# Kernel tuning notes

Measured on AMD Instinct MI355X. Metric: run time of the kernel, lower is better.

Reference implementation:

```python
import jax, jax.numpy as jnp
from jax import lax
import numpy as np

B, N, NF, EF, MD = 16, 128, 9, 3, 5
H, D, FF, L, O = 24, 768, 3072, 12, 128
NA, NID, NOD, NE, NS, NED = 4608, 256, 256, 1536, 512, 128
S = N + 1
EPS = 1e-5


def setup_inputs() -> dict:
    key = jax.random.key(0)
    ks = iter(jax.random.split(key, 64))
    emb_s = 0.02
    lin_s = 0.02 / np.sqrt(L)

    def nrm(shape, s):
        return jax.random.normal(next(ks), shape, jnp.float32) * s

    inp = {
        'x': jax.random.randint(next(ks), (B, N, NF), 0, NA + 1),
        'in_degree': jax.random.randint(next(ks), (B, N), 0, NID),
        'out_degree': jax.random.randint(next(ks), (B, N), 0, NOD),
        'spatial_pos': jax.random.randint(next(ks), (B, N, N), 0, NS),
        'edge_input': jax.random.randint(next(ks), (B, N, N, MD, EF), 0, NE + 1),
        'attn_bias': jnp.zeros((B, S, S), jnp.float32),
        # embeddings (padding_idx=0 rows zeroed)
        'atom_emb': nrm((NA + 1, D), emb_s).at[0].set(0.0),
        'in_deg_emb': nrm((NID, D), emb_s).at[0].set(0.0),
        'out_deg_emb': nrm((NOD, D), emb_s).at[0].set(0.0),
        'graph_token': nrm((1, D), emb_s),
        'edge_emb': nrm((NE + 1, H), emb_s).at[0].set(0.0),
        'edge_dis_emb': nrm((NED, H, H), emb_s),
        'spatial_emb': nrm((NS, H), emb_s).at[0].set(0.0),
        'virt_dist': nrm((1, H), emb_s),
        # stacked per-layer params
        'ln1_g': jnp.ones((L, D)), 'ln1_b': jnp.zeros((L, D)),
        'wq': nrm((L, D, D), lin_s), 'bq': jnp.zeros((L, D)),
        'wk': nrm((L, D, D), lin_s), 'bk': jnp.zeros((L, D)),
        'wv': nrm((L, D, D), lin_s), 'bv': jnp.zeros((L, D)),
        'wo': nrm((L, D, D), lin_s), 'bo': jnp.zeros((L, D)),
        'ln2_g': jnp.ones((L, D)), 'ln2_b': jnp.zeros((L, D)),
        'w1': nrm((L, D, FF), lin_s), 'b1': jnp.zeros((L, FF)),
        'w2': nrm((L, FF, D), lin_s), 'b2': jnp.zeros((L, D)),
        'final_g': jnp.ones((D,)), 'final_b': jnp.zeros((D,)),
        'out_w': nrm((D, O), lin_s), 'out_b': jnp.zeros((O,)),
    }
    return inp


def _ln(v, g, b):
    m = v.mean(-1, keepdims=True)
    va = ((v - m) ** 2).mean(-1, keepdims=True)
    return (v - m) / jnp.sqrt(va + EPS) * g + b


def _forward(x, in_degree, out_degree, spatial_pos, edge_input, attn_bias,
             atom_emb, in_deg_emb, out_deg_emb, graph_token,
             edge_emb, edge_dis_emb, spatial_emb, virt_dist,
             ln1_g, ln1_b, wq, bq, wk, bk, wv, bv, wo, bo,
             ln2_g, ln2_b, w1, b1, w2, b2, final_g, final_b, out_w, out_b):
    nb = x.shape[0]
    # ---- graph attn bias ----
    # spatial bias [B,H,N,N]
    sp_bias = spatial_emb[spatial_pos].transpose(0, 3, 1, 2)
    # multi-hop edge bias
    sp_ = jnp.where(spatial_pos == 0, 1, spatial_pos)
    sp_ = jnp.where(sp_ > 1, sp_ - 1, sp_)
    sp_ = jnp.clip(sp_, 0, MD)
    ei = edge_emb[edge_input].mean(-2)                       # [B,N,N,MD,H]
    eo = jnp.einsum('bijdh,dhk->bijk', ei, edge_dis_emb[:MD])
    edge_bias = (eo / sp_[..., None].astype(jnp.float32)).transpose(0, 3, 1, 2)
    t = virt_dist.reshape(1, H, 1)                           # virtual-token distance
    gab = jnp.repeat(attn_bias[:, None], H, axis=1)          # [B,H,S,S]
    gab = gab.at[:, :, 1:, 1:].add(sp_bias + edge_bias)
    gab = gab.at[:, :, 1:, 0].add(t)
    gab = gab.at[:, :, 0, :].add(t)
    gab = gab + attn_bias[:, None]
    # ---- node features ----
    nf = atom_emb[x].sum(-2) + in_deg_emb[in_degree] + out_deg_emb[out_degree]
    h = jnp.concatenate([jnp.broadcast_to(graph_token[None], (nb, 1, D)), nf], axis=1)  # [B,S,D]
    dk = D // H
    scale = dk ** -0.5

    def step(hc, p):
        (g1, b1n, Wq, Bq, Wk, Bk, Wv, Bv, Wo, Bo, g2, b2n, W1, B1, W2, B2) = p
        y = _ln(hc, g1, b1n)
        q = (y @ Wq + Bq).reshape(nb, S, H, dk).transpose(0, 2, 1, 3) * scale
        k = (y @ Wk + Bk).reshape(nb, S, H, dk).transpose(0, 2, 1, 3)
        v = (y @ Wv + Bv).reshape(nb, S, H, dk).transpose(0, 2, 1, 3)
        att = jnp.einsum('bhqd,bhkd->bhqk', q, k) + gab
        att = jax.nn.softmax(att, axis=-1)
        ctx = jnp.einsum('bhqk,bhkd->bhqd', att, v)
        ctx = ctx.transpose(0, 2, 1, 3).reshape(nb, S, D)
        hc = hc + (ctx @ Wo + Bo)
        y = _ln(hc, g2, b2n)
        y = jax.nn.gelu(y @ W1 + B1, approximate=False) @ W2 + B2
        return hc + y, None

    h, _ = lax.scan(step, h, (ln1_g, ln1_b, wq, bq, wk, bk, wv, bv, wo, bo,
                              ln2_g, ln2_b, w1, b1, w2, b2))
    h = _ln(h, final_g, final_b)
    return h[:, 0] @ out_w + out_b  # [B,O]


def reference(x, in_degree, out_degree, spatial_pos, edge_input, attn_bias,
              atom_emb, in_deg_emb, out_deg_emb, graph_token,
              edge_emb, edge_dis_emb, spatial_emb, virt_dist,
              ln1_g, ln1_b, wq, bq, wk, bk, wv, bv, wo, bo,
              ln2_g, ln2_b, w1, b1, w2, b2, final_g, final_b, out_w, out_b):
    return _forward(x, in_degree, out_degree, spatial_pos, edge_input, attn_bias,
                    atom_emb, in_deg_emb, out_deg_emb, graph_token,
                    edge_emb, edge_dis_emb, spatial_emb, virt_dist,
                    ln1_g, ln1_b, wq, bq, wk, bk, wv, bv, wo, bo,
                    ln2_g, ln2_b, w1, b1, w2, b2, final_g, final_b, out_w, out_b)
```

## Files before the change

kernel.cpp:

```cpp
#include <hip/hip_runtime.h>
#include <hip/hip_bf16.h>
#include <math.h>

typedef __hip_bfloat16 bf16;
typedef __attribute__((ext_vector_type(8))) short short8;
typedef __attribute__((ext_vector_type(4))) short short4v;
typedef __attribute__((ext_vector_type(4))) float f32x4;

constexpr int NB = 16;
constexpr int ND = 128;
constexpr int SQ = 129;
constexpr int NH = 24;
constexpr int DM = 768;
constexpr int DF = 3072;
constexpr int NLAY = 12;
constexpr int MROWS = NB * SQ;

__device__ __forceinline__ short f2bs(float f) {
  bf16 h = __float2bfloat16(f);
  return *(short*)&h;
}

__device__ __forceinline__ void gload16(const void* g, void* lds) {
  __builtin_amdgcn_global_load_lds(
      (const __attribute__((address_space(1))) unsigned int*)g,
      (__attribute__((address_space(3))) unsigned int*)lds, 16, 0, 0);
}

__global__ void k_nodefeat(const int* __restrict__ x, const int* __restrict__ ind,
                           const int* __restrict__ outd,
                           const float* __restrict__ atom, const float* __restrict__ ide,
                           const float* __restrict__ ode, const float* __restrict__ gtok,
                           float* __restrict__ h) {
  int bs = blockIdx.x;
  int b = bs / SQ, s = bs % SQ;
  int t = threadIdx.x;
  float* hrow = h + (size_t)bs * DM;
  if (s == 0) {
    for (int c = t; c < DM; c += 256) hrow[c] = gtok[c];
  } else {
    int n = s - 1;
    const int* xr = x + (b * ND + n) * 9;
    int a0 = xr[0], a1 = xr[1], a2 = xr[2], a3 = xr[3], a4 = xr[4];
    int a5 = xr[5], a6 = xr[6], a7 = xr[7], a8 = xr[8];
    int ii = ind[b * ND + n], oo = outd[b * ND + n];
    for (int c = t; c < DM; c += 256) {
      float acc = ide[(size_t)ii * DM + c] + ode[(size_t)oo * DM + c];
      acc += atom[(size_t)a0 * DM + c];
      acc += atom[(size_t)a1 * DM + c];
      acc += atom[(size_t)a2 * DM + c];
      acc += atom[(size_t)a3 * DM + c];
      acc += atom[(size_t)a4 * DM + c];
      acc += atom[(size_t)a5 * DM + c];
      acc += atom[(size_t)a6 * DM + c];
      acc += atom[(size_t)a7 * DM + c];
      acc += atom[(size_t)a8 * DM + c];
      hrow[c] = acc;
    }
  }
}

__global__ void k_gab_border(const float* __restrict__ ab, const float* __restrict__ virt,
                             float* __restrict__ gab) {
  int b = blockIdx.x;
  const int tot = NH * SQ + NH * ND;
  for (int idx = threadIdx.x; idx < tot; idx += 256) {
    if (idx < NH * SQ) {
      int hh = idx / SQ, j = idx % SQ;
      float v = 2.f * ab[((size_t)b * SQ + 0) * SQ + j] + virt[hh];
      gab[(((size_t)b * NH + hh) * SQ + 0) * SQ + j] = v;
    } else {
      int r = idx - NH * SQ;
      int hh = r / ND, i = r % ND + 1;
      float v = 2.f * ab[((size_t)b * SQ + i) * SQ + 0] + virt[hh];
      gab[(((size_t)b * NH + hh) * SQ + i) * SQ + 0] = v;
    }
  }
}

__global__ __launch_bounds__(256) void k_gab_edge(
    const int* __restrict__ spos, const int* __restrict__ eidx,
    const float* __restrict__ eemb, const float* __restrict__ edemb,
    const float* __restrict__ semb, const float* __restrict__ ab,
    float* __restrict__ gab) {
  __shared__ int eidxs[960];
  __shared__ short ei2[64 * 136];
  __shared__ short edT[32 * 136];
  __shared__ float ot[24][65];
  __shared__ float rinvA[64], a2A[64];
  __shared__ int spA[64];
  int bi = blockIdx.x;
  int half = bi & 1;
  int i = (bi >> 1) & 127;
  int b = bi >> 8;
  int j0 = half * 64;
  int t = threadIdx.x;
  const size_t rowbase = ((size_t)(b * ND + i)) * ND + j0;

  const int* esrc = eidx + rowbase * 15;
  for (int idx = t; idx < 960; idx += 256) eidxs[idx] = esrc[idx];
  for (int u = t; u < 720; u += 256) {
    int dh = u / 6, kq = u % 6;
    f32x4 v = *(const f32x4*)&edemb[dh * 24 + kq * 4];
    edT[(kq * 4 + 0) * 136 + dh] = f2bs(v[0]);
    edT[(kq * 4 + 1) * 136 + dh] = f2bs(v[1]);
    edT[(kq * 4 + 2) * 136 + dh] = f2bs(v[2]);
    edT[(kq * 4 + 3) * 136 + dh] = f2bs(v[3]);
  }
  for (int u = t; u < 1472; u += 256) {
    int k, dh;
    if (u < 384) { k = u >> 4; dh = 120 + (u & 15); }
    else { int v = u - 384; k = 24 + v / 136; dh = v % 136; }
    edT[k * 136 + dh] = 0;
  }
  if (t < 64) {
    int j = t;
    int sp = spos[rowbase + j];
    int spc = (sp == 0) ? 1 : sp;
    spc = (spc > 1) ? spc - 1 : spc;
    if (spc > 5) spc = 5;
    spA[j] = sp;
    rinvA[j] = 1.f / (float)spc;
    a2A[j] = 2.f * ab[((size_t)b * SQ + (i + 1)) * SQ + (j0 + j + 1)];
  }
  __syncthreads();

  {
    int j = t & 63, d = t >> 6;
#pragma unroll
    for (int pass = 0; pass < 2; pass++) {
      if (pass == 1) {
        if (t >= 64) break;
        j = t; d = 4;
      }
      const int* ep = &eidxs[j * 15 + d * 3];
      const float* r0 = eemb + (size_t)ep[0] * NH;
      const float* r1 = eemb + (size_t)ep[1] * NH;
      const float* r2 = eemb + (size_t)ep[2] * NH;
#pragma unroll
      for (int hq = 0; hq < 6; hq++) {
        f32x4 s = (*(const f32x4*)&r0[hq * 4] + *(const f32x4*)&r1[hq * 4] +
                   *(const f32x4*)&r2[hq * 4]) * (1.f / 3.f);
        short4v o;
        o[0] = f2bs(s[0]); o[1] = f2bs(s[1]); o[2] = f2bs(s[2]); o[3] = f2bs(s[3]);
        *(short4v*)&ei2[j * 136 + d * 24 + hq * 4] = o;
      }
    }
  }
  for (int idx = t; idx < 64 * 8; idx += 256) {
    int j = idx >> 3;
    ei2[j * 136 + 120 + (idx & 7)] = 0;
  }
  __syncthreads();

  int lane = t & 63, w = t >> 6;
  int fr = lane & 15, q = lane >> 4, fo = q * 8;
  f32x4 acc0 = {0.f, 0.f, 0.f, 0.f}, acc1 = {0.f, 0.f, 0.f, 0.f};
#pragma unroll
  for (int kk = 0; kk < 4; kk++) {
    short8 af = *(const short8*)&ei2[(w * 16 + fr) * 136 + kk * 32 + fo];
    short8 b0 = *(const short8*)&edT[(fr) * 136 + kk * 32 + fo];
    short8 b1 = *(const short8*)&edT[(16 + fr) * 136 + kk * 32 + fo];
    acc0 = __builtin_amdgcn_mfma_f32_16x16x32_bf16(af, b0, acc0, 0, 0, 0);
    acc1 = __builtin_amdgcn_mfma_f32_16x16x32_bf16(af, b1, acc1, 0, 0, 0);
  }
#pragma unroll
  for (int e = 0; e < 4; e++) {
    int j = w * 16 + q * 4 + e;
    ot[fr][j] = acc0[e];
    if (fr < 8) ot[16 + fr][j] = acc1[e];
  }
  __syncthreads();
  size_t obase = (((size_t)b * NH) * SQ + (i + 1)) * SQ + (j0 + 1);
  for (int idx = t; idx < 24 * 64; idx += 256) {
    int k = idx >> 6, j = idx & 63;
    float v = a2A[j] + semb[spA[j] * NH + k] + ot[k][j] * rinvA[j];
    gab[obase + (size_t)k * SQ * SQ + j] = v;
  }
}

struct Ptrs4 { const float* p[4]; };

template <int NW>
__global__ void k_transpose(Ptrs4 ps, short* __restrict__ dst, int R, int C,
                            size_t sstride) {
  __shared__ short tile[64][68];
  int z = blockIdx.z;
  const float* src = ps.p[z % NW] + (size_t)(z / NW) * sstride;
  short* d = dst + (size_t)z * (size_t)R * C;
  int r0 = blockIdx.x * 64, c0 = blockIdx.y * 64;
  int t = threadIdx.x;
  int tr = t >> 4, tc = (t & 15) * 4;
#pragma unroll
  for (int i = 0; i < 4; i++) {
    int r = tr + i * 16;
    f32x4 v = *(const f32x4*)(src + (size_t)(r0 + r) * C + c0 + tc);
    tile[r][tc + 0] = f2bs(v[0]);
    tile[r][tc + 1] = f2bs(v[1]);
    tile[r][tc + 2] = f2bs(v[2]);
    tile[r][tc + 3] = f2bs(v[3]);
  }
  __syncthreads();
#pragma unroll
  for (int i = 0; i < 4; i++) {
    int rr = tr + i * 16;
    short4v o;
    o[0] = tile[tc + 0][rr];
    o[1] = tile[tc + 1][rr];
    o[2] = tile[tc + 2][rr];
    o[3] = tile[tc + 3][rr];
    *(short4v*)(d + (size_t)(c0 + rr) * R + r0 + tc) = o;
  }
}

__global__ void k_ln(const float* __restrict__ h, const float* __restrict__ g,
                     const float* __restrict__ bb, bf16* __restrict__ y) {
  int r = blockIdx.x;
  int t = threadIdx.x, lane = t & 63, wid = t >> 6;
  __shared__ float red[8];
  const float* row = h + (size_t)r * DM;
  float v0 = row[t], v1 = row[t + 256], v2 = row[t + 512];
  float s = v0 + v1 + v2;
#pragma unroll
  for (int o = 32; o > 0; o >>= 1) s += __shfl_xor(s, o);
  if (lane == 0) red[wid] = s;
  __syncthreads();
  float mean = (red[0] + red[1] + red[2] + red[3]) * (1.f / 768.f);
  float d0 = v0 - mean, d1 = v1 - mean, d2 = v2 - mean;
  float q = d0 * d0 + d1 * d1 + d2 * d2;
#pragma unroll
  for (int o = 32; o > 0; o >>= 1) q += __shfl_xor(q, o);
  if (lane == 0) red[4 + wid] = q;
  __syncthreads();
  float var = (red[4] + red[5] + red[6] + red[7]) * (1.f / 768.f);
  float rstd = rsqrtf(var + 1e-5f);
  bf16* yr = y + (size_t)r * DM;
  yr[t] = __float2bfloat16(d0 * rstd * g[t] + bb[t]);
  yr[t + 256] = __float2bfloat16(d1 * rstd * g[t + 256] + bb[t + 256]);
  yr[t + 512] = __float2bfloat16(d2 * rstd * g[t + 512] + bb[t + 512]);
}

__global__ void k_ln_add2(float* __restrict__ h, const float* __restrict__ p0,
                          const float* __restrict__ p1, const float* __restrict__ cb,
                          const float* __restrict__ g, const float* __restrict__ bb,
                          bf16* __restrict__ y) {
  int r = blockIdx.x;
  int t = threadIdx.x, lane = t & 63, wid = t >> 6;
  __shared__ float red[8];
  size_t base = (size_t)r * DM;
  float v0 = h[base + t] + p0[base + t] + p1[base + t] + cb[t];
  float v1 = h[base + t + 256] + p0[base + t + 256] + p1[base + t + 256] + cb[t + 256];
  float v2 = h[base + t + 512] + p0[base + t + 512] + p1[base + t + 512] + cb[t + 512];
  h[base + t] = v0;
  h[base + t + 256] = v1;
  h[base + t + 512] = v2;
  float s = v0 + v1 + v2;
#pragma unroll
  for (int o = 32; o > 0; o >>= 1) s += __shfl_xor(s, o);
  if (lane == 0) red[wid] = s;
  __syncthreads();
  float mean = (red[0] + red[1] + red[2] + red[3]) * (1.f / 768.f);
  float d0 = v0 - mean, d1 = v1 - mean, d2 = v2 - mean;
  float q = d0 * d0 + d1 * d1 + d2 * d2;
#pragma unroll
  for (int o = 32; o > 0; o >>= 1) q += __shfl_xor(q, o);
  if (lane == 0) red[4 + wid] = q;
  __syncthreads();
  float var = (red[4] + red[5] + red[6] + red[7]) * (1.f / 768.f);
  float rstd = rsqrtf(var + 1e-5f);
  bf16* yr = y + base;
  yr[t] = __float2bfloat16(d0 * rstd * g[t] + bb[t]);
  yr[t + 256] = __float2bfloat16(d1 * rstd * g[t + 256] + bb[t + 256]);
  yr[t + 512] = __float2bfloat16(d2 * rstd * g[t + 512] + bb[t + 512]);
}

struct GemmPtrs {
  const short* bt[3];
  const float* bias[3];
  void* out[3];
  int aoff[3];
};

template <int MODE>
__device__ __forceinline__ void gemm_store(void* outp, size_t idx, float v) {
  if (MODE == 0 || MODE == 3) {
    ((float*)outp)[idx] = v;
  } else if (MODE == 4) {
    ((bf16*)outp)[idx] = __float2bfloat16(v);
  } else {
    float gg = 0.5f * v * (1.f + erff(v * 0.70710678118654752f));
    ((bf16*)outp)[idx] = __float2bfloat16(gg);
  }
}

template <int MODE>
__global__ __launch_bounds__(256, 2) void k_gemm128(const short* __restrict__ A, GemmPtrs p,
                                                    int M, int N, int K, int lda, int ldb) {
  __shared__ short At[2][128 * 64];
  __shared__ short Bt[2][128 * 64];
  int z = blockIdx.z;
  const short* BT = p.bt[z];
  const float* bias = p.bias[z];
  A += p.aoff[z];
  int m0 = blockIdx.x * 128, n0 = blockIdx.y * 128;
  int t = threadIdx.x, lane = t & 63, wid = t >> 6;
  int wr = wid >> 1, wc = wid & 1;
  f32x4 acc[4][4];
#pragma unroll
  for (int a = 0; a < 4; a++)
#pragma unroll
    for (int c = 0; c < 4; c++) acc[a][c] = (f32x4){0.f, 0.f, 0.f, 0.f};

  int lrow8 = lane >> 3;
  int lseg = (lane & 7) ^ lrow8;
  const short* gA[4];
  const short* gB[4];
#pragma unroll
  for (int i = 0; i < 4; i++) {
    int ar = m0 + wid * 32 + i * 8 + lrow8;
    if (ar >= M) ar = M - 1;
    gA[i] = A + (size_t)ar * lda + lseg * 8;
    int br = n0 + wid * 32 + i * 8 + lrow8;
    gB[i] = BT + (size_t)br * ldb + lseg * 8;
  }

  const int NIT = K >> 6;
#pragma unroll
  for (int i = 0; i < 4; i++) {
    gload16(gA[i], &At[0][(wid * 32 + i * 8) * 64]);
    gload16(gB[i], &Bt[0][(wid * 32 + i * 8) * 64]);
  }
  __syncthreads();

  int fr = lane & 15, q = lane >> 4;
  for (int it = 0; it < NIT; ++it) {
    int cur = it & 1;
    if (it + 1 < NIT) {
      int nxt = cur ^ 1;
      int k0 = (it + 1) << 6;
#pragma unroll
      for (int i = 0; i < 4; i++) {
        gload16(gA[i] + k0, &At[nxt][(wid * 32 + i * 8) * 64]);
        gload16(gB[i] + k0, &Bt[nxt][(wid * 32 + i * 8) * 64]);
      }
    }
    const short* Ab = At[cur];
    const short* Bb = Bt[cur];
#pragma unroll
    for (int kk = 0; kk < 2; kk++) {
      int sg = ((q + kk * 4) ^ (fr & 7)) * 8;
      short8 af[4], bf[4];
#pragma unroll
      for (int mr = 0; mr < 4; mr++)
        af[mr] = *(const short8*)&Ab[(wr * 64 + mr * 16 + fr) * 64 + sg];
#pragma unroll
      for (int nc = 0; nc < 4; nc++)
        bf[nc] = *(const short8*)&Bb[(wc * 64 + nc * 16 + fr) * 64 + sg];
#pragma unroll
      for (int mr = 0; mr < 4; mr++)
#pragma unroll
        for (int nc = 0; nc < 4; nc++)
          acc[mr][nc] = __builtin_amdgcn_mfma_f32_16x16x32_bf16(af[mr], bf[nc], acc[mr][nc], 0, 0, 0);
    }
    __syncthreads();
  }

  int rsub = q * 4;
#pragma unroll
  for (int nc = 0; nc < 4; nc++) {
    int col = n0 + wc * 64 + nc * 16 + fr;
    float bv = (MODE == 3) ? 0.f : bias[col];
#pragma unroll
    for (int mr = 0; mr < 4; mr++) {
#pragma unroll
      for (int e = 0; e < 4; e++) {
        int r = m0 + wr * 64 + mr * 16 + rsub + e;
        if (r < M) gemm_store<MODE>(p.out[z], (size_t)r * N + col, acc[mr][nc][e] + bv);
      }
    }
  }
}

template <int MODE>
__global__ __launch_bounds__(256, 3) void k_gemm64(const short* __restrict__ A, GemmPtrs p,
                                                   int M, int N, int K, int lda, int ldb) {
  __shared__ short At[2][64 * 64];
  __shared__ short Bt[2][128 * 64];
  int z = blockIdx.z;
  const short* BT = p.bt[z];
  const float* bias = p.bias[z];
  A += p.aoff[z];
  int m0 = blockIdx.x * 64, n0 = blockIdx.y * 128;
  int t = threadIdx.x, lane = t & 63, wid = t >> 6;
  int wr = wid >> 1, wc = wid & 1;
  f32x4 acc[2][4];
#pragma unroll
  for (int a = 0; a < 2; a++)
#pragma unroll
    for (int c = 0; c < 4; c++) acc[a][c] = (f32x4){0.f, 0.f, 0.f, 0.f};

  int lrow8 = lane >> 3;
  int lseg = (lane & 7) ^ lrow8;
  const short* gA[2];
  const short* gB[4];
#pragma unroll
  for (int i = 0; i < 2; i++) {
    int ar = m0 + wid * 16 + i * 8 + lrow8;
    if (ar >= M) ar = M - 1;
    gA[i] = A + (size_t)ar * lda + lseg * 8;
  }
#pragma unroll
  for (int i = 0; i < 4; i++) {
    int br = n0 + wid * 32 + i * 8 + lrow8;
    gB[i] = BT + (size_t)br * ldb + lseg * 8;
  }

  const int NIT = K >> 6;
#pragma unroll
  for (int i = 0; i < 2; i++) gload16(gA[i], &At[0][(wid * 16 + i * 8) * 64]);
#pragma unroll
  for (int i = 0; i < 4; i++) gload16(gB[i], &Bt[0][(wid * 32 + i * 8) * 64]);
  __syncthreads();

  int fr = lane & 15, q = lane >> 4;
  for (int it = 0; it < NIT; ++it) {
    int cur = it & 1;
    if (it + 1 < NIT) {
      int nxt = cur ^ 1;
      int k0 = (it + 1) << 6;
#pragma unroll
      for (int i = 0; i < 2; i++) gload16(gA[i] + k0, &At[nxt][(wid * 16 + i * 8) * 64]);
#pragma unroll
      for (int i = 0; i < 4; i++) gload16(gB[i] + k0, &Bt[nxt][(wid * 32 + i * 8) * 64]);
    }
    const short* Ab = At[cur];
    const short* Bb = Bt[cur];
#pragma unroll
    for (int kk = 0; kk < 2; kk++) {
      int sg = ((q + kk * 4) ^ (fr & 7)) * 8;
      short8 af[2], bf[4];
#pragma unroll
      for (int mr = 0; mr < 2; mr++)
        af[mr] = *(const short8*)&Ab[(wr * 32 + mr * 16 + fr) * 64 + sg];
#pragma unroll
      for (int nc = 0; nc < 4; nc++)
        bf[nc] = *(const short8*)&Bb[(wc * 64 + nc * 16 + fr) * 64 + sg];
#pragma unroll
      for (int mr = 0; mr < 2; mr++)
#pragma unroll
        for (int nc = 0; nc < 4; nc++)
          acc[mr][nc] = __builtin_amdgcn_mfma_f32_16x16x32_bf16(af[mr], bf[nc], acc[mr][nc], 0, 0, 0);
    }
    __syncthreads();
  }

  int rsub = q * 4;
#pragma unroll
  for (int nc = 0; nc < 4; nc++) {
    int col = n0 + wc * 64 + nc * 16 + fr;
    float bv = (MODE == 3) ? 0.f : bias[col];
#pragma unroll
    for (int mr = 0; mr < 2; mr++) {
#pragma unroll
      for (int e = 0; e < 4; e++) {
        int r = m0 + wr * 32 + mr * 16 + rsub + e;
        if (r < M) gemm_store<MODE>(p.out[z], (size_t)r * N + col, acc[mr][nc][e] + bv);
      }
    }
  }
}

__global__ __launch_bounds__(256) void k_attn(const bf16* __restrict__ Q,
                                              const bf16* __restrict__ Kb,
                                              const bf16* __restrict__ Vb,
                                              const float* __restrict__ gab,
                                              bf16* __restrict__ ctx) {
  __shared__ short Ql[144 * 40];
  __shared__ short Kl[144 * 40];
  __shared__ short Vt[32 * 168];
  __shared__ short Pc[144 * 40];
  int bh = blockIdx.x;
  int b = bh / NH, hh = bh % NH;
  int t = threadIdx.x;
  for (int idx = t; idx < 32 * 40; idx += 256) {
    int d = idx / 40, kk = 128 + (idx % 40);
    Vt[d * 168 + kk] = 0;
  }
  for (int idx = t; idx < 129 * 4; idx += 256) {
    int s = idx >> 2, seg = idx & 3;
    size_t src = ((size_t)(b * SQ + s)) * DM + hh * 32 + seg * 8;
    *(short8*)&Ql[s * 40 + seg * 8] = *(const short8*)((const short*)Q + src);
    *(short8*)&Kl[s * 40 + seg * 8] = *(const short8*)((const short*)Kb + src);
  }
  for (int idx = t; idx < 15 * 4; idx += 256) {
    int s = 129 + (idx >> 2), seg = idx & 3;
    short8 zz = {0, 0, 0, 0, 0, 0, 0, 0};
    *(short8*)&Ql[s * 40 + seg * 8] = zz;
    *(short8*)&Kl[s * 40 + seg * 8] = zz;
  }
  for (int idx = t; idx < 129 * 4; idx += 256) {
    int kk = idx >> 2, seg = idx & 3;
    size_t src = ((size_t)(b * SQ + kk)) * DM + hh * 32 + seg * 8;
    short8 v = *(const short8*)((const short*)Vb + src);
#pragma unroll
    for (int j = 0; j < 8; j++) Vt[(seg * 8 + j) * 168 + kk] = v[j];
  }
  __syncthreads();

  int lane = t & 63, w = t >> 6;
  int c16 = lane & 15, q4 = lane >> 4;
  const float scale = 0.17677669529663689f;
  const float* gabp = gab + (((size_t)(b * NH + hh)) * SQ) * SQ;

  for (int mt = w; mt < 9; mt += 4) {
    f32x4 sc[9];
    short8 aq = *(const short8*)&Ql[(mt * 16 + c16) * 40 + q4 * 8];
#pragma unroll
    for (int nt = 0; nt < 9; nt++) {
      short8 bk = *(const short8*)&Kl[(nt * 16 + c16) * 40 + q4 * 8];
      f32x4 zz = {0.f, 0.f, 0.f, 0.f};
      sc[nt] = __builtin_amdgcn_mfma_f32_16x16x32_bf16(aq, bk, zz, 0, 0, 0);
    }
#pragma unroll
    for (int e = 0; e < 4; e++) {
      int row = mt * 16 + q4 * 4 + e;
      int rr = row < 129 ? row : 128;
      const float* grow = gabp + (size_t)rr * SQ;
      float mloc = -1e30f;
#pragma unroll
      for (int nt = 0; nt < 9; nt++) {
        int col = nt * 16 + c16;
        float s = (col < 129) ? (sc[nt][e] * scale + grow[col]) : -1e30f;
        sc[nt][e] = s;
        mloc = fmaxf(mloc, s);
      }
#pragma unroll
      for (int o = 1; o < 16; o <<= 1) mloc = fmaxf(mloc, __shfl_xor(mloc, o));
      float sum = 0.f;
#pragma unroll
      for (int nt = 0; nt < 9; nt++) {
        float pp = __expf(sc[nt][e] - mloc);
        sc[nt][e] = pp;
        sum += pp;
      }
#pragma unroll
      for (int o = 1; o < 16; o <<= 1) sum += __shfl_xor(sum, o);
      float inv = 1.f / sum;
#pragma unroll
      for (int nt = 0; nt < 9; nt++) sc[nt][e] *= inv;
    }
    f32x4 oacc0 = {0.f, 0.f, 0.f, 0.f}, oacc1 = {0.f, 0.f, 0.f, 0.f};
#pragma unroll
    for (int c = 0; c < 5; c++) {
#pragma unroll
      for (int u = 0; u < 2; u++) {
        int nt = c * 2 + u;
        if (nt < 9) {
#pragma unroll
          for (int e = 0; e < 4; e++)
            Pc[(mt * 16 + q4 * 4 + e) * 40 + u * 16 + c16] = f2bs(sc[nt][e]);
        } else {
#pragma unroll
          for (int e = 0; e < 4; e++)
            Pc[(mt * 16 + q4 * 4 + e) * 40 + u * 16 + c16] = 0;
        }
      }
      asm volatile("s_waitcnt lgkmcnt(0)" ::: "memory");
      __builtin_amdgcn_sched_barrier(0);
      short8 ap = *(const short8*)&Pc[(mt * 16 + c16) * 40 + q4 * 8];
      short8 bv0 = *(const short8*)&Vt[(c16) * 168 + c * 32 + q4 * 8];
      short8 bv1 = *(const short8*)&Vt[(16 + c16) * 168 + c * 32 + q4 * 8];
      oacc0 = __builtin_amdgcn_mfma_f32_16x16x32_bf16(ap, bv0, oacc0, 0, 0, 0);
      oacc1 = __builtin_amdgcn_mfma_f32_16x16x32_bf16(ap, bv1, oacc1, 0, 0, 0);
    }
#pragma unroll
    for (int e = 0; e < 4; e++) {
      int row = mt * 16 + q4 * 4 + e;
      if (row < 129) {
        size_t obase = ((size_t)(b * SQ + row)) * DM + hh * 32;
        ctx[obase + c16] = __float2bfloat16(oacc0[e]);
        ctx[obase + 16 + c16] = __float2bfloat16(oacc1[e]);
      }
    }
  }
}

__global__ void k_final_add2(const float* __restrict__ h, const float* __restrict__ p0,
                             const float* __restrict__ p1, const float* __restrict__ cb,
                             const float* __restrict__ g, const float* __restrict__ bb,
                             const float* __restrict__ ow, const float* __restrict__ ob,
                             float* __restrict__ out) {
  int b = blockIdx.x;
  int t = threadIdx.x, lane = t & 63, wid = t >> 6;
  __shared__ float red[8];
  __shared__ float yn[768];
  size_t base = (size_t)(b * SQ) * DM;
  float v0 = h[base + t] + p0[base + t] + p1[base + t] + cb[t];
  float v1 = h[base + t + 256] + p0[base + t + 256] + p1[base + t + 256] + cb[t + 256];
  float v2 = h[base + t + 512] + p0[base + t + 512] + p1[base + t + 512] + cb[t + 512];
  float s = v0 + v1 + v2;
#pragma unroll
  for (int o = 32; o > 0; o >>= 1) s += __shfl_xor(s, o);
  if (lane == 0) red[wid] = s;
  __syncthreads();
  float mean = (red[0] + red[1] + red[2] + red[3]) * (1.f / 768.f);
  float d0 = v0 - mean, d1 = v1 - mean, d2 = v2 - mean;
  float q = d0 * d0 + d1 * d1 + d2 * d2;
#pragma unroll
  for (int o = 32; o > 0; o >>= 1) q += __shfl_xor(q, o);
  if (lane == 0) red[4 + wid] = q;
  __syncthreads();
  float var = (red[4] + red[5] + red[6] + red[7]) * (1.f / 768.f);
  float rstd = rsqrtf(var + 1e-5f);
  yn[t] = d0 * rstd * g[t] + bb[t];
  yn[t + 256] = d1 * rstd * g[t + 256] + bb[t + 256];
  yn[t + 512] = d2 * rstd * g[t + 512] + bb[t + 512];
  __syncthreads();
  if (t < 128) {
    float acc = ob[t];
    for (int d = 0; d < 768; d++) acc += yn[d] * ow[d * 128 + t];
    out[b * 128 + t] = acc;
  }
}

extern "C" void kernel_launch(void* const* d_in, const int* in_sizes, int n_in,
                              void* d_out, int out_size, void* d_ws, size_t ws_size,
                              hipStream_t stream) {
  (void)in_sizes; (void)n_in; (void)out_size;
  const int* x     = (const int*)d_in[0];
  const int* ind   = (const int*)d_in[1];
  const int* outd  = (const int*)d_in[2];
  const int* spos  = (const int*)d_in[3];
  const int* eidx  = (const int*)d_in[4];
  const float* ab   = (const float*)d_in[5];
  const float* atom = (const float*)d_in[6];
  const float* ide  = (const float*)d_in[7];
  const float* ode  = (const float*)d_in[8];
  const float* gtok = (const float*)d_in[9];
  const float* eemb = (const float*)d_in[10];
  const float* edemb= (const float*)d_in[11];
  const float* semb = (const float*)d_in[12];
  const float* virt = (const float*)d_in[13];
  const float* ln1g = (const float*)d_in[14];
  const float* ln1b = (const float*)d_in[15];
  const float* wq  = (const float*)d_in[16];
  const float* bq   = (const float*)d_in[17];
  const float* wk  = (const float*)d_in[18];
  const float* bk   = (const float*)d_in[19];
  const float* wv  = (const float*)d_in[20];
  const float* bv   = (const float*)d_in[21];
  const float* wo  = (const float*)d_in[22];
  const float* bo   = (const float*)d_in[23];
  const float* ln2g = (const float*)d_in[24];
  const float* ln2b = (const float*)d_in[25];
  const float* w1  = (const float*)d_in[26];
  const float* b1   = (const float*)d_in[27];
  const float* w2  = (const float*)d_in[28];
  const float* b2   = (const float*)d_in[29];
  const float* fg   = (const float*)d_in[30];
  const float* fb   = (const float*)d_in[31];
  const float* ow   = (const float*)d_in[32];
  const float* ob   = (const float*)d_in[33];
  float* out = (float*)d_out;

  const int DD2 = DM * DM;
  const size_t WQKVO = (size_t)DD2;
  const size_t WFF = (size_t)DM * DF;

  char* ws = (char*)d_ws;
  size_t off = 0;
  auto alloc = [&](size_t bytes) -> void* {
    void* p = ws + off;
    off += (bytes + 255) & ~(size_t)255;
    return p;
  };
  float* gab = (float*)alloc((size_t)NB * NH * SQ * SQ * 4);
  float* h   = (float*)alloc((size_t)MROWS * DM * 4);
  bf16* y    = (bf16*)alloc((size_t)MROWS * DM * 2);
  bf16* qb   = (bf16*)alloc((size_t)MROWS * DM * 2);
  bf16* kb2  = (bf16*)alloc((size_t)MROWS * DM * 2);
  bf16* vb2  = (bf16*)alloc((size_t)MROWS * DM * 2);
  bf16* ctx  = (bf16*)alloc((size_t)MROWS * DM * 2);
  bf16* t1   = (bf16*)alloc((size_t)MROWS * DF * 2);
  float* p0  = (float*)alloc((size_t)MROWS * DM * 4);
  float* p1  = (float*)alloc((size_t)MROWS * DM * 4);

  size_t need_hoist = off + ((size_t)NLAY * 4 * WQKVO + 2 * (size_t)NLAY * WFF) * 2 + (1 << 20);
  bool hoist = ws_size >= need_hoist;
  short* wT  = (short*)alloc((hoist ? (size_t)NLAY * 4 * WQKVO : 4 * WQKVO) * 2);
  short* w1T = (short*)alloc((hoist ? (size_t)NLAY * WFF : WFF) * 2);
  short* w2T = (short*)alloc((hoist ? (size_t)NLAY * WFF : WFF) * 2);

  dim3 blk(256);
  k_nodefeat<<<dim3(NB * SQ), blk, 0, stream>>>(x, ind, outd, atom, ide, ode, gtok, h);
  k_gab_border<<<dim3(NB), blk, 0, stream>>>(ab, virt, gab);
  k_gab_edge<<<dim3(NB * ND * 2), blk, 0, stream>>>(spos, eidx, eemb, edemb, semb, ab, gab);

  if (hoist) {
    Ptrs4 pq; pq.p[0] = wq; pq.p[1] = wk; pq.p[2] = wv; pq.p[3] = wo;
    k_transpose<4><<<dim3(12, 12, 48), blk, 0, stream>>>(pq, wT, DM, DM, WQKVO);
    Ptrs4 pa; pa.p[0] = w1; pa.p[1] = pa.p[2] = pa.p[3] = w1;
    k_transpose<1><<<dim3(12, 48, 12), blk, 0, stream>>>(pa, w1T, DM, DF, WFF);
    Ptrs4 pb; pb.p[0] = w2; pb.p[1] = pb.p[2] = pb.p[3] = w2;
    k_transpose<1><<<dim3(48, 12, 12), blk, 0, stream>>>(pb, w2T, DF, DM, WFF);
  }

  for (int l = 0; l < NLAY; l++) {
    if (!hoist) {
      Ptrs4 pq;
      pq.p[0] = wq + (size_t)l * DD2; pq.p[1] = wk + (size_t)l * DD2;
      pq.p[2] = wv + (size_t)l * DD2; pq.p[3] = wo + (size_t)l * DD2;
      k_transpose<4><<<dim3(12, 12, 4), blk, 0, stream>>>(pq, wT, DM, DM, 0);
      Ptrs4 pa; pa.p[0] = w1 + (size_t)l * WFF; pa.p[1] = pa.p[2] = pa.p[3] = pa.p[0];
      k_transpose<1><<<dim3(12, 48, 1), blk, 0, stream>>>(pa, w1T, DM, DF, 0);
      Ptrs4 pb; pb.p[0] = w2 + (size_t)l * WFF; pb.p[1] = pb.p[2] = pb.p[3] = pb.p[0];
      k_transpose<1><<<dim3(48, 12, 1), blk, 0, stream>>>(pb, w2T, DF, DM, 0);
    }
    const short* wTl  = wT  + (hoist ? (size_t)l * 4 * WQKVO : 0);
    const short* w1Tl = w1T + (hoist ? (size_t)l * WFF : 0);
    const short* w2Tl = w2T + (hoist ? (size_t)l * WFF : 0);

    if (l == 0)
      k_ln<<<dim3(MROWS), blk, 0, stream>>>(h, ln1g, ln1b, y);

    GemmPtrs gq;
    gq.bt[0] = wTl; gq.bt[1] = wTl + DD2; gq.bt[2] = wTl + 2 * DD2;
    gq.bias[0] = bq + l * DM; gq.bias[1] = bk + l * DM; gq.bias[2] = bv + l * DM;
    gq.out[0] = qb; gq.out[1] = kb2; gq.out[2] = vb2;
    gq.aoff[0] = gq.aoff[1] = gq.aoff[2] = 0;
    k_gemm128<4><<<dim3(17, 6, 3), blk, 0, stream>>>((const short*)y, gq, MROWS, DM, DM, DM, DM);

    k_attn<<<dim3(NB * NH), blk, 0, stream>>>(qb, kb2, vb2, gab, ctx);

    GemmPtrs go;
    go.bt[0] = wTl + 3 * DD2; go.bt[1] = wTl + 3 * DD2 + 384;
    go.bias[0] = go.bias[1] = nullptr;
    go.out[0] = p0; go.out[1] = p1;
    go.aoff[0] = 0; go.aoff[1] = 384;
    go.bt[2] = go.bt[0]; go.out[2] = p0; go.aoff[2] = 0; go.bias[2] = nullptr;
    k_gemm64<3><<<dim3(33, 6, 2), blk, 0, stream>>>((const short*)ctx, go, MROWS, DM, 384, DM, DM);

    k_ln_add2<<<dim3(MROWS), blk, 0, stream>>>(h, p0, p1, bo + l * DM,
                                               ln2g + l * DM, ln2b + l * DM, y);

    GemmPtrs g1;
    g1.bt[0] = g1.bt[1] = g1.bt[2] = w1Tl;
    g1.bias[0] = g1.bias[1] = g1.bias[2] = b1 + l * DF;
    g1.out[0] = g1.out[1] = g1.out[2] = t1;
    g1.aoff[0] = g1.aoff[1] = g1.aoff[2] = 0;
    k_gemm128<2><<<dim3(17, 24, 1), blk, 0, stream>>>((const short*)y, g1, MROWS, DF, DM, DM, DM);

    GemmPtrs g2;
    g2.bt[0] = w2Tl; g2.bt[1] = w2Tl + 1536;
    g2.bias[0] = g2.bias[1] = nullptr;
    g2.out[0] = p0; g2.out[1] = p1;
    g2.aoff[0] = 0; g2.aoff[1] = 1536;
    g2.bt[2] = g2.bt[0]; g2.out[2] = p0; g2.aoff[2] = 0; g2.bias[2] = nullptr;
    k_gemm64<3><<<dim3(33, 6, 2), blk, 0, stream>>>((const short*)t1, g2, MROWS, DM, 1536, DF, DF);

    if (l < NLAY - 1) {
      k_ln_add2<<<dim3(MROWS), blk, 0, stream>>>(h, p0, p1, b2 + l * DM,
                                                 ln1g + (l + 1) * DM, ln1b + (l + 1) * DM, y);
    } else {
      k_final_add2<<<dim3(NB), blk, 0, stream>>>(h, p0, p1, b2 + l * DM, fg, fb, ow, ob, out);
    }
  }
}
```

Baseline: 1.702 ms.

## Replace double-buffered LDS GEMM tiles with single buffer to raise occupancy

Both GEMM kernels drop the LDS ping-pong buffers and the prefetch of the next K-tile. Each iteration now loads one tile, syncs, and computes, so LDS use is halved and the launch bounds ask for one more block per CU. The aim is to hide global-load latency with more resident blocks instead of software pipelining. In exchange, load and compute within a block no longer overlap.

```diff
diff --git a/kernel.cpp b/kernel.cpp
--- a/kernel.cpp
+++ b/kernel.cpp
@@ -294,10 +294,10 @@
 }
 
 template <int MODE>
-__global__ __launch_bounds__(256, 2) void k_gemm128(const short* __restrict__ A, GemmPtrs p,
+__global__ __launch_bounds__(256, 3) void k_gemm128(const short* __restrict__ A, GemmPtrs p,
                                                     int M, int N, int K, int lda, int ldb) {
-  __shared__ short At[2][128 * 64];
-  __shared__ short Bt[2][128 * 64];
+  __shared__ short At[128 * 64];
+  __shared__ short Bt[128 * 64];
   int z = blockIdx.z;
   const short* BT = p.bt[z];
   const float* bias = p.bias[z];
@@ -325,37 +325,25 @@
   }
 
   const int NIT = K >> 6;
-#pragma unroll
-  for (int i = 0; i < 4; i++) {
-    gload16(gA[i], &At[0][(wid * 32 + i * 8) * 64]);
-    gload16(gB[i], &Bt[0][(wid * 32 + i * 8) * 64]);
-  }
-  __syncthreads();
-
   int fr = lane & 15, q = lane >> 4;
   for (int it = 0; it < NIT; ++it) {
-    int cur = it & 1;
-    if (it + 1 < NIT) {
-      int nxt = cur ^ 1;
-      int k0 = (it + 1) << 6;
-#pragma unroll
-      for (int i = 0; i < 4; i++) {
-        gload16(gA[i] + k0, &At[nxt][(wid * 32 + i * 8) * 64]);
-        gload16(gB[i] + k0, &Bt[nxt][(wid * 32 + i * 8) * 64]);
-      }
-    }
-    const short* Ab = At[cur];
-    const short* Bb = Bt[cur];
+    int k0 = it << 6;
+#pragma unroll
+    for (int i = 0; i < 4; i++) {
+      gload16(gA[i] + k0, &At[(wid * 32 + i * 8) * 64]);
+      gload16(gB[i] + k0, &Bt[(wid * 32 + i * 8) * 64]);
+    }
+    __syncthreads();
 #pragma unroll
     for (int kk = 0; kk < 2; kk++) {
       int sg = ((q + kk * 4) ^ (fr & 7)) * 8;
       short8 af[4], bf[4];
 #pragma unroll
       for (int mr = 0; mr < 4; mr++)
-        af[mr] = *(const short8*)&Ab[(wr * 64 + mr * 16 + fr) * 64 + sg];
+        af[mr] = *(const short8*)&At[(wr * 64 + mr * 16 + fr) * 64 + sg];
 #pragma unroll
       for (int nc = 0; nc < 4; nc++)
-        bf[nc] = *(const short8*)&Bb[(wc * 64 + nc * 16 + fr) * 64 + sg];
+        bf[nc] = *(const short8*)&Bt[(wc * 64 + nc * 16 + fr) * 64 + sg];
 #pragma unroll
       for (int mr = 0; mr < 4; mr++)
 #pragma unroll
@@ -382,10 +370,10 @@
 }
 
 template <int MODE>
-__global__ __launch_bounds__(256, 3) void k_gemm64(const short* __restrict__ A, GemmPtrs p,
+__global__ __launch_bounds__(256, 4) void k_gemm64(const short* __restrict__ A, GemmPtrs p,
                                                    int M, int N, int K, int lda, int ldb) {
-  __shared__ short At[2][64 * 64];
-  __shared__ short Bt[2][128 * 64];
+  __shared__ short At[64 * 64];
+  __shared__ short Bt[128 * 64];
   int z = blockIdx.z;
   const short* BT = p.bt[z];
   const float* bias = p.bias[z];
@@ -416,35 +404,24 @@
   }
 
   const int NIT = K >> 6;
-#pragma unroll
-  for (int i = 0; i < 2; i++) gload16(gA[i], &At[0][(wid * 16 + i * 8) * 64]);
-#pragma unroll
-  for (int i = 0; i < 4; i++) gload16(gB[i], &Bt[0][(wid * 32 + i * 8) * 64]);
-  __syncthreads();
-
   int fr = lane & 15, q = lane >> 4;
   for (int it = 0; it < NIT; ++it) {
-    int cur = it & 1;
-    if (it + 1 < NIT) {
-      int nxt = cur ^ 1;
-      int k0 = (it + 1) << 6;
-#pragma unroll
-      for (int i = 0; i < 2; i++) gload16(gA[i] + k0, &At[nxt][(wid * 16 + i * 8) * 64]);
-#pragma unroll
-      for (int i = 0; i < 4; i++) gload16(gB[i] + k0, &Bt[nxt][(wid * 32 + i * 8) * 64]);
-    }
-    const short* Ab = At[cur];
-    const short* Bb = Bt[cur];
+    int k0 = it << 6;
+#pragma unroll
+    for (int i = 0; i < 2; i++) gload16(gA[i] + k0, &At[(wid * 16 + i * 8) * 64]);
+#pragma unroll
+    for (int i = 0; i < 4; i++) gload16(gB[i] + k0, &Bt[(wid * 32 + i * 8) * 64]);
+    __syncthreads();
 #pragma unroll
     for (int kk = 0; kk < 2; kk++) {
       int sg = ((q + kk * 4) ^ (fr & 7)) * 8;
       short8 af[2], bf[4];
 #pragma unroll
       for (int mr = 0; mr < 2; mr++)
-        af[mr] = *(const short8*)&Ab[(wr * 32 + mr * 16 + fr) * 64 + sg];
+        af[mr] = *(const short8*)&At[(wr * 32 + mr * 16 + fr) * 64 + sg];
 #pragma unroll
       for (int nc = 0; nc < 4; nc++)
-        bf[nc] = *(const short8*)&Bb[(wc * 64 + nc * 16 + fr) * 64 + sg];
+        bf[nc] = *(const short8*)&Bt[(wc * 64 + nc * 16 + fr) * 64 + sg];
 #pragma unroll
       for (int mr = 0; mr < 2; mr++)
 #pragma unroll
```

After: 1.698 ms. About the same (-0.3%).
